# Kernel tuning notes

Measured on AMD Instinct MI355X. Metric: run time of the kernel, lower is better.

Reference implementation:

```python
import jax, jax.numpy as jnp
import numpy as np

CONF_THRESH = 0.25


def setup_inputs() -> dict:
    key = jax.random.key(0)
    # Raw YOLO head output: [batch, n_anchors, 4 box + 1 objectness + 80 classes]
    output = jax.random.uniform(key, (16, 25200, 85), dtype=jnp.float32)
    return {"output": output}


def reference(output):
    # Faithful JAX version of ModelWrapper._process_raw_output fallback path.
    # Torch emits a variable-length [M, 6] tensor; with static shapes we emit
    # the dense [B, N, 6] decoded boxes with below-threshold rows zeroed
    # (equivalent information: masked rows are exactly the dropped ones).
    box_xy = output[..., 0:2]            # [B, N, 2]
    box_wh = output[..., 2:4]            # [B, N, 2]
    box_conf = output[..., 4]            # [B, N]
    box_cls = output[..., 5:]            # [B, N, C]

    half_wh = box_wh * 0.5
    xy_min = box_xy - half_wh            # xmin, ymin
    xy_max = box_xy + half_wh            # xmax, ymax

    max_scores = jnp.max(box_cls, axis=-1)                    # [B, N]
    max_cls_idx = jnp.argmax(box_cls, axis=-1)                # [B, N]
    scores = box_conf * max_scores                            # [B, N]
    mask = scores > CONF_THRESH                               # [B, N]

    boxes = jnp.concatenate(
        [xy_min, xy_max, scores[..., None],
         max_cls_idx.astype(output.dtype)[..., None]], axis=-1)  # [B, N, 6]
    return jnp.where(mask[..., None], boxes, jnp.zeros((), dtype=output.dtype))
```

## Files before the change

kernel.cpp:

```cpp
#include <hip/hip_runtime.h>

#define ROWS_PER_BLOCK 64
#define THREADS 64
#define ROW_F 85
#define NCLS 80
#define CONF_THRESH 0.25f

#define TILE_F (ROWS_PER_BLOCK * ROW_F)
#define TILE_V (TILE_F / 4)
#define PER_THREAD 21
#define TAIL_V (TILE_V - PER_THREAD * THREADS)

__global__ __launch_bounds__(THREADS) void yolo_post_kernel(
    const float* __restrict__ in, float* __restrict__ out, int nrows) {
  __shared__ float tile[TILE_F];

  const long long row0 = (long long)blockIdx.x * ROWS_PER_BLOCK;
  const long long base_f = row0 * ROW_F;
  const long long total_f = (long long)nrows * ROW_F;

  const float4* __restrict__ src = (const float4*)(in + base_f);
  float4* dstv = (float4*)tile;
  const int t = threadIdx.x;

  if (base_f + TILE_F <= total_f) {
    float4 v[PER_THREAD];
#pragma unroll
    for (int k = 0; k < PER_THREAD; ++k) {
      v[k] = src[t + k * THREADS];
    }
    float4 extra;
    if (t < TAIL_V) {
      extra = src[PER_THREAD * THREADS + t];
    }
#pragma unroll
    for (int k = 0; k < PER_THREAD; ++k) {
      dstv[t + k * THREADS] = v[k];
    }
    if (t < TAIL_V) {
      dstv[PER_THREAD * THREADS + t] = extra;
    }
  } else {
    for (int i = t; i < TILE_V; i += THREADS) {
      if (base_f + (long long)i * 4 + 3 < total_f) dstv[i] = src[i];
    }
  }
  __syncthreads();

  const long long r = row0 + t;
  if (r >= nrows) return;
  const float* row = tile + t * ROW_F;

  float cx = row[0];
  float cy = row[1];
  float hw = row[2] * 0.5f;
  float hh = row[3] * 0.5f;
  float conf = row[4];

  float best = row[5];
  int bidx = 0;
#pragma unroll
  for (int c = 1; c < NCLS; ++c) {
    float v = row[5 + c];
    bool gt = v > best;
    best = gt ? v : best;
    bidx = gt ? c : bidx;
  }

  float score = conf * best;
  bool keep = score > CONF_THRESH;

  float o0 = keep ? cx - hw : 0.0f;
  float o1 = keep ? cy - hh : 0.0f;
  float o2 = keep ? cx + hw : 0.0f;
  float o3 = keep ? cy + hh : 0.0f;
  float o4 = keep ? score : 0.0f;
  float o5 = keep ? (float)bidx : 0.0f;

  float* op = out + r * 6;
  op[0] = o0;
  op[1] = o1;
  op[2] = o2;
  op[3] = o3;
  op[4] = o4;
  op[5] = o5;
}

extern "C" void kernel_launch(void* const* d_in, const int* in_sizes, int n_in,
                              void* d_out, int out_size, void* d_ws, size_t ws_size,
                              hipStream_t stream) {
  const float* in = (const float*)d_in[0];
  float* out = (float*)d_out;
  const int nrows = in_sizes[0] / ROW_F;
  const int grid = (nrows + ROWS_PER_BLOCK - 1) / ROWS_PER_BLOCK;
  yolo_post_kernel<<<grid, THREADS, 0, stream>>>(in, out, nrows);
}
```

Measured before the change: 192.1 us.

## Process several tiles per block with register prefetch of the next tile

Each block now handles four 64-row tiles in sequence. While the current tile is reduced from LDS, the next tile's global loads are issued into registers and written to LDS afterwards, overlapping memory latency with the argmax compute. The block-wide barrier is dropped because the block is a single 64-lane wavefront, and outputs are written as float2 pairs. The trade-off is a grid four times smaller, which lowers the number of waves in flight for latency hiding, plus higher register pressure.

```diff
diff --git a/kernel.cpp b/kernel.cpp
--- a/kernel.cpp
+++ b/kernel.cpp
@@ -1,89 +1,118 @@
 #include <hip/hip_runtime.h>
 
-#define ROWS_PER_BLOCK 64
+#define ROWS_PER_TILE 64
 #define THREADS 64
 #define ROW_F 85
 #define NCLS 80
 #define CONF_THRESH 0.25f
 
-#define TILE_F (ROWS_PER_BLOCK * ROW_F)
+#define TILE_F (ROWS_PER_TILE * ROW_F)
 #define TILE_V (TILE_F / 4)
 #define PER_THREAD 21
 #define TAIL_V (TILE_V - PER_THREAD * THREADS)
+#define TILES_PER_BLOCK 4
 
 __global__ __launch_bounds__(THREADS) void yolo_post_kernel(
-    const float* __restrict__ in, float* __restrict__ out, int nrows) {
+    const float* __restrict__ in, float* __restrict__ out, long long nrows) {
   __shared__ float tile[TILE_F];
-
-  const long long row0 = (long long)blockIdx.x * ROWS_PER_BLOCK;
-  const long long base_f = row0 * ROW_F;
-  const long long total_f = (long long)nrows * ROW_F;
-
-  const float4* __restrict__ src = (const float4*)(in + base_f);
   float4* dstv = (float4*)tile;
   const int t = threadIdx.x;
 
-  if (base_f + TILE_F <= total_f) {
-    float4 v[PER_THREAD];
+  const long long full_tiles = nrows / ROWS_PER_TILE;
+  const long long ntiles = (nrows + ROWS_PER_TILE - 1) / ROWS_PER_TILE;
+  long long ti = (long long)blockIdx.x * TILES_PER_BLOCK;
+  long long ti_end = ti + TILES_PER_BLOCK;
+  if (ti_end > ntiles) ti_end = ntiles;
+  if (ti >= ti_end) return;
+  long long full_end = ti_end < full_tiles ? ti_end : full_tiles;
+
+  float4 v[PER_THREAD];
+  float4 extra;
+
+  if (ti < full_end) {
+    {
+      const float4* __restrict__ src = (const float4*)(in + ti * TILE_F);
 #pragma unroll
-    for (int k = 0; k < PER_THREAD; ++k) {
-      v[k] = src[t + k * THREADS];
-    }
-    float4 extra;
-    if (t < TAIL_V) {
-      extra = src[PER_THREAD * THREADS + t];
+      for (int k = 0; k < PER_THREAD; ++k) v[k] = src[t + k * THREADS];
+      if (t < TAIL_V) extra = src[PER_THREAD * THREADS + t];
     }
 #pragma unroll
-    for (int k = 0; k < PER_THREAD; ++k) {
-      dstv[t + k * THREADS] = v[k];
-    }
-    if (t < TAIL_V) {
-      dstv[PER_THREAD * THREADS + t] = extra;
-    }
-  } else {
-    for (int i = t; i < TILE_V; i += THREADS) {
-      if (base_f + (long long)i * 4 + 3 < total_f) dstv[i] = src[i];
+    for (int k = 0; k < PER_THREAD; ++k) dstv[t + k * THREADS] = v[k];
+    if (t < TAIL_V) dstv[PER_THREAD * THREADS + t] = extra;
+
+    while (ti < full_end) {
+      const long long nxt = ti + 1;
+      const bool have_next = nxt < full_end;
+      if (have_next) {
+        const float4* __restrict__ src = (const float4*)(in + nxt * TILE_F);
+#pragma unroll
+        for (int k = 0; k < PER_THREAD; ++k) v[k] = src[t + k * THREADS];
+        if (t < TAIL_V) extra = src[PER_THREAD * THREADS + t];
+      }
+
+      const long long r = ti * ROWS_PER_TILE + t;
+      const float* row = tile + t * ROW_F;
+      float cx = row[0];
+      float cy = row[1];
+      float hw = row[2] * 0.5f;
+      float hh = row[3] * 0.5f;
+      float conf = row[4];
+      float best = row[5];
+      int bidx = 0;
+#pragma unroll
+      for (int c = 1; c < NCLS; ++c) {
+        float x = row[5 + c];
+        bool g = x > best;
+        best = g ? x : best;
+        bidx = g ? c : bidx;
+      }
+      float score = conf * best;
+      bool keep = score > CONF_THRESH;
+      float2 o01 = keep ? make_float2(cx - hw, cy - hh) : make_float2(0.f, 0.f);
+      float2 o23 = keep ? make_float2(cx + hw, cy + hh) : make_float2(0.f, 0.f);
+      float2 o45 = keep ? make_float2(score, (float)bidx) : make_float2(0.f, 0.f);
+      float2* op = (float2*)(out + r * 6);
+      op[0] = o01;
+      op[1] = o23;
+      op[2] = o45;
+
+      if (have_next) {
+#pragma unroll
+        for (int k = 0; k < PER_THREAD; ++k) dstv[t + k * THREADS] = v[k];
+        if (t < TAIL_V) dstv[PER_THREAD * THREADS + t] = extra;
+      }
+      ti = nxt;
     }
   }
-  __syncthreads();
 
-  const long long r = row0 + t;
-  if (r >= nrows) return;
-  const float* row = tile + t * ROW_F;
-
-  float cx = row[0];
-  float cy = row[1];
-  float hw = row[2] * 0.5f;
-  float hh = row[3] * 0.5f;
-  float conf = row[4];
-
-  float best = row[5];
-  int bidx = 0;
-#pragma unroll
-  for (int c = 1; c < NCLS; ++c) {
-    float v = row[5 + c];
-    bool gt = v > best;
-    best = gt ? v : best;
-    bidx = gt ? c : bidx;
+  if (ti < ti_end) {
+    const long long r = ti * ROWS_PER_TILE + t;
+    if (r < nrows) {
+      const float* __restrict__ row = in + r * ROW_F;
+      float cx = row[0];
+      float cy = row[1];
+      float hw = row[2] * 0.5f;
+      float hh = row[3] * 0.5f;
+      float conf = row[4];
+      float best = row[5];
+      int bidx = 0;
+      for (int c = 1; c < NCLS; ++c) {
+        float x = row[5 + c];
+        bool g = x > best;
+        best = g ? x : best;
+        bidx = g ? c : bidx;
+      }
+      float score = conf * best;
+      bool keep = score > CONF_THRESH;
+      float* op = out + r * 6;
+      op[0] = keep ? cx - hw : 0.0f;
+      op[1] = keep ? cy - hh : 0.0f;
+      op[2] = keep ? cx + hw : 0.0f;
+      op[3] = keep ? cy + hh : 0.0f;
+      op[4] = keep ? score : 0.0f;
+      op[5] = keep ? (float)bidx : 0.0f;
+    }
   }
-
-  float score = conf * best;
-  bool keep = score > CONF_THRESH;
-
-  float o0 = keep ? cx - hw : 0.0f;
-  float o1 = keep ? cy - hh : 0.0f;
-  float o2 = keep ? cx + hw : 0.0f;
-  float o3 = keep ? cy + hh : 0.0f;
-  float o4 = keep ? score : 0.0f;
-  float o5 = keep ? (float)bidx : 0.0f;
-
-  float* op = out + r * 6;
-  op[0] = o0;
-  op[1] = o1;
-  op[2] = o2;
-  op[3] = o3;
-  op[4] = o4;
-  op[5] = o5;
 }
 
 extern "C" void kernel_launch(void* const* d_in, const int* in_sizes, int n_in,
@@ -91,7 +120,8 @@
                               hipStream_t stream) {
   const float* in = (const float*)d_in[0];
   float* out = (float*)d_out;
-  const int nrows = in_sizes[0] / ROW_F;
-  const int grid = (nrows + ROWS_PER_BLOCK - 1) / ROWS_PER_BLOCK;
+  const long long nrows = (long long)in_sizes[0] / ROW_F;
+  const long long ntiles = (nrows + ROWS_PER_TILE - 1) / ROWS_PER_TILE;
+  const int grid = (int)((ntiles + TILES_PER_BLOCK - 1) / TILES_PER_BLOCK);
   yolo_post_kernel<<<grid, THREADS, 0, stream>>>(in, out, nrows);
 }
```

Result: slower. 224.1 us (+16.7%).
